# Kernel optimization log

Measured on AMD Instinct MI355X. Metric: run time of the kernel, lower is better.

The kernel has to match this reference:

```python
import jax, jax.numpy as jnp
import numpy as np

WS, OV, NH, CH = 16, 4, 6, 96
HD = CH // NH
SCALE = HD ** -0.5
EPS = 1e-5


def setup_inputs() -> dict:
    key = jax.random.key(0)
    ks = jax.random.split(key, 6)
    x = jax.random.normal(ks[0], (1, CH, 256, 256), jnp.float32)
    wq = jax.random.normal(ks[1], (CH, CH), jnp.float32) * 0.02      # torch Linear weight [out,in]
    wkv = jax.random.normal(ks[2], (2 * CH, CH), jnp.float32) * 0.02
    wproj = jax.random.normal(ks[3], (CH, CH), jnp.float32) * 0.02
    gamma = 1.0 + 0.02 * jax.random.normal(ks[4], (CH,), jnp.float32)
    beta = 0.02 * jax.random.normal(ks[5], (CH,), jnp.float32)
    return dict(x=x, wq=wq, wkv=wkv, wproj=wproj, gamma=gamma, beta=beta)


def reference(x, wq, wkv, wproj, gamma, beta):
    B, C, H, W = x.shape
    ws, ov, nh, hd = WS, OV, NH, HD
    ph = (ws - H % ws) % ws
    pw = (ws - W % ws) % ws
    xp = jnp.pad(x, ((0, 0), (0, 0), (0, ph), (0, pw)), mode='reflect') if (ph or pw) else x
    Hp, Wp = xp.shape[2], xp.shape[3]
    nhw, nww = Hp // ws, Wp // ws
    # non-overlapping query windows: (B*nW, ws*ws, C)
    xhw = xp.transpose(0, 2, 3, 1)  # B,Hp,Wp,C
    xwin = (xhw.reshape(B, nhw, ws, nww, ws, C)
                .transpose(0, 1, 3, 2, 4, 5)
                .reshape(B * nhw * nww, ws * ws, C))
    # LayerNorm (biased variance, eps=1e-5) then Q projection
    mu = xwin.mean(-1, keepdims=True)
    var = xwin.var(-1, keepdims=True)
    xn = (xwin - mu) / jnp.sqrt(var + EPS) * gamma + beta
    q = xn @ wq.T  # (Bw, ws*ws, C)
    # overlapping halo windows via gather (equiv. of pad + unfold)
    ws_ov = ws + 2 * ov
    xp2 = jnp.pad(xp, ((0, 0), (0, 0), (ov, ov), (ov, ov)), mode='reflect')
    ih = (jnp.arange(nhw) * ws)[:, None] + jnp.arange(ws_ov)[None, :]  # (nhw, ws_ov)
    iw = (jnp.arange(nww) * ws)[:, None] + jnp.arange(ws_ov)[None, :]  # (nww, ws_ov)
    xuf = xp2[:, :, ih[:, :, None, None], iw[None, None, :, :]]  # B,C,nhw,ws_ov,nww,ws_ov
    xuf = xuf.transpose(0, 2, 4, 3, 5, 1).reshape(B * nhw * nww, ws_ov * ws_ov, C)
    # KV projection and head split
    kv = (xuf @ wkv.T).reshape(-1, ws_ov * ws_ov, 2, nh, hd)
    k = kv[:, :, 0].transpose(0, 2, 1, 3)  # (Bw, nh, L2, hd)
    v = kv[:, :, 1].transpose(0, 2, 1, 3)
    qh = q.reshape(-1, ws * ws, nh, hd).transpose(0, 2, 1, 3)  # (Bw, nh, L1, hd)
    attn = jax.nn.softmax(jnp.einsum('bhqd,bhkd->bhqk', qh, k) * SCALE, axis=-1)
    out = jnp.einsum('bhqk,bhkd->bhqd', attn, v).transpose(0, 2, 1, 3).reshape(-1, ws * ws, C)
    out = out @ wproj.T + xwin
    out = (out.reshape(B, nhw, nww, ws, ws, C)
               .transpose(0, 1, 3, 2, 4, 5)
               .reshape(B, Hp, Wp, C)
               .transpose(0, 3, 1, 2))
    return out[:, :, :H, :W]
```

## Files before the change

kernel.cpp:

```cpp
#include <hip/hip_runtime.h>

#define NPIX 65536
#define HD 16
#define NTOK 576
#define QS 0.36067376022f
#define XPAD 100

typedef short s16x4 __attribute__((ext_vector_type(4)));
typedef short s16x8 __attribute__((ext_vector_type(8)));
typedef float f32x4 __attribute__((ext_vector_type(4)));

#define MFMA32(A, B, Cc) __builtin_amdgcn_mfma_f32_16x16x32_bf16((A), (B), (Cc), 0, 0, 0)

static __device__ __forceinline__ unsigned short f2b_rne(float f) {
    unsigned u = __builtin_bit_cast(unsigned, f);
    unsigned r = u + 0x7fffu + ((u >> 16) & 1u);
    return (unsigned short)(r >> 16);
}
static __device__ __forceinline__ float fexp2(float x) {
#if defined(__has_builtin)
#if __has_builtin(__builtin_amdgcn_exp2f)
    return __builtin_amdgcn_exp2f(x);
#else
    return exp2f(x);
#endif
#else
    return exp2f(x);
#endif
}
static __device__ __forceinline__ unsigned pkbf(float hi, float lo) {
#if defined(__has_builtin)
#if __has_builtin(__builtin_amdgcn_perm)
    return __builtin_amdgcn_perm(__builtin_bit_cast(unsigned, hi),
                                 __builtin_bit_cast(unsigned, lo), 0x07060302u);
#else
    return (__builtin_bit_cast(unsigned, hi) & 0xffff0000u) |
           (__builtin_bit_cast(unsigned, lo) >> 16);
#endif
#else
    return (__builtin_bit_cast(unsigned, hi) & 0xffff0000u) |
           (__builtin_bit_cast(unsigned, lo) >> 16);
#endif
}
static __device__ __forceinline__ int reflect_idx(int p) {
    p = (p < 0) ? -p : p;
    p = (p > 255) ? (510 - p) : p;
    return p;
}

__global__ __launch_bounds__(256) void prep_w(const float* __restrict__ wq,
                                              const float* __restrict__ wkv,
                                              const float* __restrict__ wproj,
                                              unsigned short* __restrict__ wB,
                                              unsigned short* __restrict__ wpB) {
    int idx = blockIdx.x * 256 + threadIdx.x;
    if (idx < 27648) {
        float v = (idx < 9216) ? wq[idx] : wkv[idx - 9216];
        wB[idx] = f2b_rne(v);
    } else {
        wpB[idx - 27648] = f2b_rne(wproj[idx - 27648]);
    }
}

__global__ __launch_bounds__(256, 2) void lnqkv(const float* __restrict__ x,
                                                const unsigned short* __restrict__ wB,
                                                const float* __restrict__ gamma,
                                                const float* __restrict__ beta,
                                                unsigned short* __restrict__ qwin,
                                                unsigned short* __restrict__ kmap,
                                                unsigned short* __restrict__ vmap) {
    __shared__ unsigned short xq[64][XPAD];
    __shared__ unsigned short xkv[64][XPAD];
    __shared__ float ps[4][64], pss[4][64];
    const int tid = threadIdx.x, lane = tid & 63, w = tid >> 6;
    const int p0 = blockIdx.x * 64;

    float xv[24];
    float s = 0.f, ss = 0.f;
#pragma unroll
    for (int i = 0; i < 24; ++i) {
        float v = x[(size_t)(w * 24 + i) * NPIX + p0 + lane];
        xv[i] = v; s += v; ss += v * v;
    }
    ps[w][lane] = s; pss[w][lane] = ss;
    __syncthreads();
    float st = 0.f, sst = 0.f;
#pragma unroll
    for (int q = 0; q < 4; ++q) { st += ps[q][lane]; sst += pss[q][lane]; }
    float mu = st * (1.0f / 96.0f);
    float var = sst * (1.0f / 96.0f) - mu * mu;
    float rs = rsqrtf(var + 1e-5f);
#pragma unroll
    for (int i = 0; i < 24; i += 2) {
        int c = w * 24 + i;
        float n0 = (xv[i] - mu) * rs * gamma[c] + beta[c];
        float n1 = (xv[i + 1] - mu) * rs * gamma[c + 1] + beta[c + 1];
        unsigned pq = (unsigned)f2b_rne(n0) | ((unsigned)f2b_rne(n1) << 16);
        *(unsigned*)&xq[lane][c] = pq;
        unsigned pk = (unsigned)f2b_rne(xv[i]) | ((unsigned)f2b_rne(xv[i + 1]) << 16);
        *(unsigned*)&xkv[lane][c] = pk;
    }
    __syncthreads();

    const int cq = lane & 15, g = lane >> 4;
    const int prow = w * 16 + cq;

    s16x8 bq[3], bkv[3];
#pragma unroll
    for (int ks = 0; ks < 3; ++ks) {
        int off = ks * 32 + g * 8;
        s16x4 lo = *(const s16x4*)&xq[prow][off];
        s16x4 hi = *(const s16x4*)&xq[prow][off + 4];
        bq[ks] = s16x8{lo[0], lo[1], lo[2], lo[3], hi[0], hi[1], hi[2], hi[3]};
        s16x4 lo2 = *(const s16x4*)&xkv[prow][off];
        s16x4 hi2 = *(const s16x4*)&xkv[prow][off + 4];
        bkv[ks] = s16x8{lo2[0], lo2[1], lo2[2], lo2[3], hi2[0], hi2[1], hi2[2], hi2[3]};
    }

    f32x4 acc[18];
#pragma unroll
    for (int t = 0; t < 18; ++t) acc[t] = f32x4{0.f, 0.f, 0.f, 0.f};
#pragma unroll
    for (int t = 0; t < 18; ++t) {
        const unsigned short* wrow = wB + (size_t)(t * 16 + cq) * 96 + g * 8;
        s16x8 a0 = *(const s16x8*)(wrow);
        s16x8 a1 = *(const s16x8*)(wrow + 32);
        s16x8 a2 = *(const s16x8*)(wrow + 64);
        if (t < 6) {
            acc[t] = MFMA32(a0, bq[0], acc[t]);
            acc[t] = MFMA32(a1, bq[1], acc[t]);
            acc[t] = MFMA32(a2, bq[2], acc[t]);
        } else {
            acc[t] = MFMA32(a0, bkv[0], acc[t]);
            acc[t] = MFMA32(a1, bkv[1], acc[t]);
            acc[t] = MFMA32(a2, bkv[2], acc[t]);
        }
    }

    const int p = p0 + prow;
    const int y = p >> 8, xx = p & 255;
    const int win = (y >> 4) * 16 + (xx >> 4);
    const int tok = (y & 15) * 16 + (xx & 15);
#pragma unroll
    for (int t = 0; t < 6; ++t) {
        union { s16x4 v; unsigned short h[4]; } u;
#pragma unroll
        for (int r = 0; r < 4; ++r) u.h[r] = f2b_rne(acc[t][r] * QS);
        *(s16x4*)(qwin + (size_t)(win * 256 + tok) * 96 + t * 16 + g * 4) = u.v;
    }
#pragma unroll
    for (int t = 6; t < 18; ++t) {
        int h = (t < 12) ? (t - 6) : (t - 12);
        unsigned short* base = (t < 12) ? kmap : vmap;
        union { s16x4 v; unsigned short h4[4]; } u;
#pragma unroll
        for (int r = 0; r < 4; ++r) u.h4[r] = f2b_rne(acc[t][r]);
        *(s16x4*)(base + (size_t)h * NPIX * HD + (size_t)p * HD + g * 4) = u.v;
    }
}

__global__ __launch_bounds__(256, 4) void attn_k(const unsigned short* __restrict__ qwin,
                                                 const unsigned short* __restrict__ kmap,
                                                 const unsigned short* __restrict__ vmap,
                                                 unsigned short* __restrict__ attn2) {
    __shared__ __align__(16) unsigned short vT_lds[16][580];
    __shared__ int koff[NTOK];
    const int tid = threadIdx.x;
    const int win = blockIdx.x / 6, head = blockIdx.x % 6;
    const int wi = win >> 4, wj = win & 15;

    const unsigned short* kbase = kmap + (size_t)head * NPIX * HD;
    const unsigned short* vbase = vmap + (size_t)head * NPIX * HD;
    for (int i = tid; i < NTOK; i += 256) {
        int r = i / 24, cc = i - r * 24;
        int py = reflect_idx(wi * 16 - 4 + r);
        int px = reflect_idx(wj * 16 - 4 + cc);
        int pix = py * 256 + px;
        koff[i] = pix * 32;
        const uint4* vsrc = (const uint4*)(vbase + (size_t)pix * HD);
        union { uint4 u; unsigned short h[8]; } ua, ub;
        ua.u = vsrc[0]; ub.u = vsrc[1];
#pragma unroll
        for (int d = 0; d < 8; ++d) vT_lds[d][i] = ua.h[d];
#pragma unroll
        for (int d = 0; d < 8; ++d) vT_lds[8 + d][i] = ub.h[d];
    }
    __syncthreads();

    const int lane = tid & 63, wv = tid >> 6;
    const int c = lane & 15, g = lane >> 4;
    const char* kbyte = (const char*)kbase + g * 8;

    union U8 { s16x8 v8; s16x4 v4[2]; };
    U8 qf[4];
#pragma unroll
    for (int qt = 0; qt < 4; ++qt) {
        int tok = wv * 64 + qt * 16 + c;
        qf[qt].v4[0] = *(const s16x4*)(qwin + ((size_t)(win * 256 + tok)) * 96 + head * HD + g * 4);
        qf[qt].v4[1] = s16x4{0, 0, 0, 0};
    }

    f32x4 o[4];
    float psA[4], psB[4];
#pragma unroll
    for (int qt = 0; qt < 4; ++qt) {
        o[qt] = f32x4{0.f, 0.f, 0.f, 0.f};
        psA[qt] = 0.f; psB[qt] = 0.f;
    }
    const f32x4 zero = f32x4{0.f, 0.f, 0.f, 0.f};

    U8 kf0, kf1, vf;
    kf0.v4[1] = s16x4{0, 0, 0, 0};
    kf1.v4[1] = s16x4{0, 0, 0, 0};

    for (int nt = 0; nt < 18; ++nt) {
        const int t0 = nt * 32;
        int o0 = koff[t0 + c];
        int o1 = koff[t0 + 16 + c];
        kf0.v4[0] = *(const s16x4*)(kbyte + o0);
        kf1.v4[0] = *(const s16x4*)(kbyte + o1);
        vf.v4[0] = *(const s16x4*)&vT_lds[c][t0 + g * 4];
        vf.v4[1] = *(const s16x4*)&vT_lds[c][t0 + 16 + g * 4];
#pragma unroll
        for (int qt = 0; qt < 4; ++qt) {
            f32x4 s0 = MFMA32(kf0.v8, qf[qt].v8, zero);
            f32x4 s1 = MFMA32(kf1.v8, qf[qt].v8, zero);
            float pe0 = fexp2(s0[0]), pe1 = fexp2(s0[1]);
            float pe2 = fexp2(s0[2]), pe3 = fexp2(s0[3]);
            float pe4 = fexp2(s1[0]), pe5 = fexp2(s1[1]);
            float pe6 = fexp2(s1[2]), pe7 = fexp2(s1[3]);
            psA[qt] += (pe0 + pe1) + (pe2 + pe3);
            psB[qt] += (pe4 + pe5) + (pe6 + pe7);
            union { uint4 u; s16x8 v; } bp;
            bp.u.x = pkbf(pe1, pe0);
            bp.u.y = pkbf(pe3, pe2);
            bp.u.z = pkbf(pe5, pe4);
            bp.u.w = pkbf(pe7, pe6);
            o[qt] = MFMA32(vf.v8, bp.v, o[qt]);
        }
    }

#pragma unroll
    for (int qt = 0; qt < 4; ++qt) {
        float d = psA[qt] + psB[qt];
        d += __shfl_xor(d, 16);
        d += __shfl_xor(d, 32);
        float inv = 1.0f / d;
        int tok = wv * 64 + qt * 16 + c;
        union { s16x4 v; unsigned short h[4]; } u;
#pragma unroll
        for (int r = 0; r < 4; ++r) u.h[r] = f2b_rne(o[qt][r] * inv);
        *(s16x4*)(attn2 + (size_t)(win * 256 + tok) * 96 + head * HD + g * 4) = u.v;
    }
}

__global__ __launch_bounds__(256) void proj_k(const unsigned short* __restrict__ attn2,
                                              const unsigned short* __restrict__ wpB,
                                              const float* __restrict__ x,
                                              float* __restrict__ out) {
    const int tid = threadIdx.x, lane = tid & 63, w = tid >> 6;
    const int cq = lane & 15, g = lane >> 4;
    const int p0 = blockIdx.x * 64;
    const int p = p0 + w * 16 + cq;
    const int y = p >> 8, xx = p & 255;
    const int win = (y >> 4) * 16 + (xx >> 4);
    const int tok = (y & 15) * 16 + (xx & 15);

    const unsigned short* arow = attn2 + (size_t)(win * 256 + tok) * 96 + g * 8;
    s16x8 b0 = *(const s16x8*)(arow);
    s16x8 b1 = *(const s16x8*)(arow + 32);
    s16x8 b2 = *(const s16x8*)(arow + 64);

    f32x4 acc[6];
#pragma unroll
    for (int t = 0; t < 6; ++t) acc[t] = f32x4{0.f, 0.f, 0.f, 0.f};
#pragma unroll
    for (int t = 0; t < 6; ++t) {
        const unsigned short* wrow = wpB + (size_t)(t * 16 + cq) * 96 + g * 8;
        acc[t] = MFMA32(*(const s16x8*)(wrow), b0, acc[t]);
        acc[t] = MFMA32(*(const s16x8*)(wrow + 32), b1, acc[t]);
        acc[t] = MFMA32(*(const s16x8*)(wrow + 64), b2, acc[t]);
    }
#pragma unroll
    for (int t = 0; t < 6; ++t) {
#pragma unroll
        for (int r = 0; r < 4; ++r) {
            size_t idx = (size_t)(t * 16 + 4 * g + r) * NPIX + p;
            out[idx] = acc[t][r] + x[idx];
        }
    }
}

extern "C" void kernel_launch(void* const* d_in, const int* in_sizes, int n_in,
                              void* d_out, int out_size, void* d_ws, size_t ws_size,
                              hipStream_t stream) {
    const float* x     = (const float*)d_in[0];
    const float* wq    = (const float*)d_in[1];
    const float* wkv   = (const float*)d_in[2];
    const float* wproj = (const float*)d_in[3];
    const float* gamma = (const float*)d_in[4];
    const float* beta  = (const float*)d_in[5];
    float* out = (float*)d_out;

    char* ws = (char*)d_ws;
    unsigned short* wB   = (unsigned short*)ws;
    unsigned short* wpB  = (unsigned short*)(ws + 55296);
    const size_t MAP = (size_t)NPIX * 96 * 2;
    unsigned short* qwin  = (unsigned short*)(ws + 73728);
    unsigned short* kmap  = (unsigned short*)(ws + 73728 + MAP);
    unsigned short* vmap  = (unsigned short*)(ws + 73728 + 2 * MAP);
    unsigned short* attn2 = (unsigned short*)(ws + 73728 + 3 * MAP);

    prep_w<<<144, 256, 0, stream>>>(wq, wkv, wproj, wB, wpB);
    lnqkv<<<1024, 256, 0, stream>>>(x, wB, gamma, beta, qwin, kmap, vmap);
    attn_k<<<1536, 256, 0, stream>>>(qwin, kmap, vmap, attn2);
    proj_k<<<1024, 256, 0, stream>>>(attn2, wpB, x, out);
}
```

Before: 86.11 us.

## Software-pipeline attention loop to overlap QK MFMA with exp and PV

Restructures the attention inner loop into a software pipeline. Each iteration issues the QK score MFMAs for the current tile, the PV MFMA for the previous tile, and prefetches the next tile's K and V, all before running exp/pack on the current scores. The aim is to hide MFMA and gather latency behind transcendental work. The koff and vT arrays are padded so the one-tile-ahead prefetch stays in bounds, at the cost of more registers for the buffered scores and probabilities under a 4-wave occupancy bound.

```diff
diff --git a/kernel.cpp b/kernel.cpp
--- a/kernel.cpp
+++ b/kernel.cpp
@@ -5,6 +5,7 @@
 #define NTOK 576
 #define QS 0.36067376022f
 #define XPAD 100
+#define VCOL 628
 
 typedef short s16x4 __attribute__((ext_vector_type(4)));
 typedef short s16x8 __attribute__((ext_vector_type(8)));
@@ -163,27 +164,31 @@
                                                  const unsigned short* __restrict__ kmap,
                                                  const unsigned short* __restrict__ vmap,
                                                  unsigned short* __restrict__ attn2) {
-    __shared__ __align__(16) unsigned short vT_lds[16][580];
-    __shared__ int koff[NTOK];
+    __shared__ __align__(16) unsigned short vT_lds[16][VCOL];
+    __shared__ int koff[640];
     const int tid = threadIdx.x;
     const int win = blockIdx.x / 6, head = blockIdx.x % 6;
     const int wi = win >> 4, wj = win & 15;
 
     const unsigned short* kbase = kmap + (size_t)head * NPIX * HD;
     const unsigned short* vbase = vmap + (size_t)head * NPIX * HD;
-    for (int i = tid; i < NTOK; i += 256) {
-        int r = i / 24, cc = i - r * 24;
-        int py = reflect_idx(wi * 16 - 4 + r);
-        int px = reflect_idx(wj * 16 - 4 + cc);
-        int pix = py * 256 + px;
-        koff[i] = pix * 32;
-        const uint4* vsrc = (const uint4*)(vbase + (size_t)pix * HD);
-        union { uint4 u; unsigned short h[8]; } ua, ub;
-        ua.u = vsrc[0]; ub.u = vsrc[1];
-#pragma unroll
-        for (int d = 0; d < 8; ++d) vT_lds[d][i] = ua.h[d];
-#pragma unroll
-        for (int d = 0; d < 8; ++d) vT_lds[8 + d][i] = ub.h[d];
+    for (int i = tid; i < 640; i += 256) {
+        if (i < NTOK) {
+            int r = i / 24, cc = i - r * 24;
+            int py = reflect_idx(wi * 16 - 4 + r);
+            int px = reflect_idx(wj * 16 - 4 + cc);
+            int pix = py * 256 + px;
+            koff[i] = pix * 32;
+            const uint4* vsrc = (const uint4*)(vbase + (size_t)pix * HD);
+            union { uint4 u; unsigned short h[8]; } ua, ub;
+            ua.u = vsrc[0]; ub.u = vsrc[1];
+#pragma unroll
+            for (int d = 0; d < 8; ++d) vT_lds[d][i] = ua.h[d];
+#pragma unroll
+            for (int d = 0; d < 8; ++d) vT_lds[8 + d][i] = ub.h[d];
+        } else {
+            koff[i] = 0;
+        }
     }
     __syncthreads();
 
@@ -212,33 +217,72 @@
     U8 kf0, kf1, vf;
     kf0.v4[1] = s16x4{0, 0, 0, 0};
     kf1.v4[1] = s16x4{0, 0, 0, 0};
-
-    for (int nt = 0; nt < 18; ++nt) {
-        const int t0 = nt * 32;
-        int o0 = koff[t0 + c];
-        int o1 = koff[t0 + 16 + c];
+    union BP { uint4 u; s16x8 v; } bp[4];
+
+    {
+        int o0 = koff[c], o1 = koff[16 + c];
         kf0.v4[0] = *(const s16x4*)(kbyte + o0);
         kf1.v4[0] = *(const s16x4*)(kbyte + o1);
-        vf.v4[0] = *(const s16x4*)&vT_lds[c][t0 + g * 4];
-        vf.v4[1] = *(const s16x4*)&vT_lds[c][t0 + 16 + g * 4];
+        vf.v4[0] = *(const s16x4*)&vT_lds[c][g * 4];
+        vf.v4[1] = *(const s16x4*)&vT_lds[c][16 + g * 4];
+    }
+    f32x4 s0[4], s1[4];
+#pragma unroll
+    for (int qt = 0; qt < 4; ++qt) {
+        s0[qt] = MFMA32(kf0.v8, qf[qt].v8, zero);
+        s1[qt] = MFMA32(kf1.v8, qf[qt].v8, zero);
+    }
+    {
+        int o0 = koff[32 + c], o1 = koff[48 + c];
+        kf0.v4[0] = *(const s16x4*)(kbyte + o0);
+        kf1.v4[0] = *(const s16x4*)(kbyte + o1);
+    }
+#pragma unroll
+    for (int qt = 0; qt < 4; ++qt) {
+        float pe0 = fexp2(s0[qt][0]), pe1 = fexp2(s0[qt][1]);
+        float pe2 = fexp2(s0[qt][2]), pe3 = fexp2(s0[qt][3]);
+        float pe4 = fexp2(s1[qt][0]), pe5 = fexp2(s1[qt][1]);
+        float pe6 = fexp2(s1[qt][2]), pe7 = fexp2(s1[qt][3]);
+        psA[qt] += (pe0 + pe1) + (pe2 + pe3);
+        psB[qt] += (pe4 + pe5) + (pe6 + pe7);
+        bp[qt].u.x = pkbf(pe1, pe0);
+        bp[qt].u.y = pkbf(pe3, pe2);
+        bp[qt].u.z = pkbf(pe5, pe4);
+        bp[qt].u.w = pkbf(pe7, pe6);
+    }
+
+    for (int nt = 1; nt < 18; ++nt) {
 #pragma unroll
         for (int qt = 0; qt < 4; ++qt) {
-            f32x4 s0 = MFMA32(kf0.v8, qf[qt].v8, zero);
-            f32x4 s1 = MFMA32(kf1.v8, qf[qt].v8, zero);
-            float pe0 = fexp2(s0[0]), pe1 = fexp2(s0[1]);
-            float pe2 = fexp2(s0[2]), pe3 = fexp2(s0[3]);
-            float pe4 = fexp2(s1[0]), pe5 = fexp2(s1[1]);
-            float pe6 = fexp2(s1[2]), pe7 = fexp2(s1[3]);
+            s0[qt] = MFMA32(kf0.v8, qf[qt].v8, zero);
+            s1[qt] = MFMA32(kf1.v8, qf[qt].v8, zero);
+        }
+#pragma unroll
+        for (int qt = 0; qt < 4; ++qt) o[qt] = MFMA32(vf.v8, bp[qt].v, o[qt]);
+        {
+            int o0 = koff[(nt + 1) * 32 + c], o1 = koff[(nt + 1) * 32 + 16 + c];
+            kf0.v4[0] = *(const s16x4*)(kbyte + o0);
+            kf1.v4[0] = *(const s16x4*)(kbyte + o1);
+            const int t0 = nt * 32;
+            vf.v4[0] = *(const s16x4*)&vT_lds[c][t0 + g * 4];
+            vf.v4[1] = *(const s16x4*)&vT_lds[c][t0 + 16 + g * 4];
+        }
+#pragma unroll
+        for (int qt = 0; qt < 4; ++qt) {
+            float pe0 = fexp2(s0[qt][0]), pe1 = fexp2(s0[qt][1]);
+            float pe2 = fexp2(s0[qt][2]), pe3 = fexp2(s0[qt][3]);
+            float pe4 = fexp2(s1[qt][0]), pe5 = fexp2(s1[qt][1]);
+            float pe6 = fexp2(s1[qt][2]), pe7 = fexp2(s1[qt][3]);
             psA[qt] += (pe0 + pe1) + (pe2 + pe3);
             psB[qt] += (pe4 + pe5) + (pe6 + pe7);
-            union { uint4 u; s16x8 v; } bp;
-            bp.u.x = pkbf(pe1, pe0);
-            bp.u.y = pkbf(pe3, pe2);
-            bp.u.z = pkbf(pe5, pe4);
-            bp.u.w = pkbf(pe7, pe6);
-            o[qt] = MFMA32(vf.v8, bp.v, o[qt]);
-        }
-    }
+            bp[qt].u.x = pkbf(pe1, pe0);
+            bp[qt].u.y = pkbf(pe3, pe2);
+            bp[qt].u.z = pkbf(pe5, pe4);
+            bp[qt].u.w = pkbf(pe7, pe6);
+        }
+    }
+#pragma unroll
+    for (int qt = 0; qt < 4; ++qt) o[qt] = MFMA32(vf.v8, bp[qt].v, o[qt]);
 
 #pragma unroll
     for (int qt = 0; qt < 4; ++qt) {
```

Measured after the change: 83.46 us. 3.1% less time.

## Software-pipeline K/V fragment loads in attention loop and swizzle block order

Applied to the files above, without the earlier changes.

Restructures the attention inner loop into double-buffered A/B stages that prefetch K fragments and key offsets two iterations ahead and V fragments from LDS, so global-load latency can overlap with MFMA and exp work. All score MFMAs for a stage are batched before the exponentials, and s_setprio raises wave priority around the MFMA groups. It also remaps blockIdx with an 8-way swizzle to change which windows and heads run together, and pads the LDS arrays so over-the-end prefetches read zeroed offsets and stay in bounds. The changes raise register pressure and LDS use per block, which could reduce occupancy.

```diff
diff --git a/kernel.cpp b/kernel.cpp
--- a/kernel.cpp
+++ b/kernel.cpp
@@ -5,6 +5,8 @@
 #define NTOK 576
 #define QS 0.36067376022f
 #define XPAD 100
+#define VCOL 692
+#define KOFFN 704
 
 typedef short s16x4 __attribute__((ext_vector_type(4)));
 typedef short s16x8 __attribute__((ext_vector_type(8)));
@@ -163,27 +165,32 @@
                                                  const unsigned short* __restrict__ kmap,
                                                  const unsigned short* __restrict__ vmap,
                                                  unsigned short* __restrict__ attn2) {
-    __shared__ __align__(16) unsigned short vT_lds[16][580];
-    __shared__ int koff[NTOK];
+    __shared__ __align__(16) unsigned short vT_lds[16][VCOL];
+    __shared__ int koff[KOFFN];
     const int tid = threadIdx.x;
-    const int win = blockIdx.x / 6, head = blockIdx.x % 6;
+    const int swz = (blockIdx.x & 7) * 192 + (blockIdx.x >> 3);
+    const int win = swz / 6, head = swz % 6;
     const int wi = win >> 4, wj = win & 15;
 
     const unsigned short* kbase = kmap + (size_t)head * NPIX * HD;
     const unsigned short* vbase = vmap + (size_t)head * NPIX * HD;
-    for (int i = tid; i < NTOK; i += 256) {
-        int r = i / 24, cc = i - r * 24;
-        int py = reflect_idx(wi * 16 - 4 + r);
-        int px = reflect_idx(wj * 16 - 4 + cc);
-        int pix = py * 256 + px;
-        koff[i] = pix * 32;
-        const uint4* vsrc = (const uint4*)(vbase + (size_t)pix * HD);
-        union { uint4 u; unsigned short h[8]; } ua, ub;
-        ua.u = vsrc[0]; ub.u = vsrc[1];
-#pragma unroll
-        for (int d = 0; d < 8; ++d) vT_lds[d][i] = ua.h[d];
-#pragma unroll
-        for (int d = 0; d < 8; ++d) vT_lds[8 + d][i] = ub.h[d];
+    for (int i = tid; i < KOFFN; i += 256) {
+        if (i < NTOK) {
+            int r = i / 24, cc = i - r * 24;
+            int py = reflect_idx(wi * 16 - 4 + r);
+            int px = reflect_idx(wj * 16 - 4 + cc);
+            int pix = py * 256 + px;
+            koff[i] = pix * 32;
+            const uint4* vsrc = (const uint4*)(vbase + (size_t)pix * HD);
+            union { uint4 u; unsigned short h[8]; } ua, ub;
+            ua.u = vsrc[0]; ub.u = vsrc[1];
+#pragma unroll
+            for (int d = 0; d < 8; ++d) vT_lds[d][i] = ua.h[d];
+#pragma unroll
+            for (int d = 0; d < 8; ++d) vT_lds[8 + d][i] = ub.h[d];
+        } else {
+            koff[i] = 0;
+        }
     }
     __syncthreads();
 
@@ -209,36 +216,63 @@
     }
     const f32x4 zero = f32x4{0.f, 0.f, 0.f, 0.f};
 
-    U8 kf0, kf1, vf;
-    kf0.v4[1] = s16x4{0, 0, 0, 0};
-    kf1.v4[1] = s16x4{0, 0, 0, 0};
-
-    for (int nt = 0; nt < 18; ++nt) {
-        const int t0 = nt * 32;
-        int o0 = koff[t0 + c];
-        int o1 = koff[t0 + 16 + c];
-        kf0.v4[0] = *(const s16x4*)(kbyte + o0);
-        kf1.v4[0] = *(const s16x4*)(kbyte + o1);
-        vf.v4[0] = *(const s16x4*)&vT_lds[c][t0 + g * 4];
-        vf.v4[1] = *(const s16x4*)&vT_lds[c][t0 + 16 + g * 4];
-#pragma unroll
-        for (int qt = 0; qt < 4; ++qt) {
-            f32x4 s0 = MFMA32(kf0.v8, qf[qt].v8, zero);
-            f32x4 s1 = MFMA32(kf1.v8, qf[qt].v8, zero);
-            float pe0 = fexp2(s0[0]), pe1 = fexp2(s0[1]);
-            float pe2 = fexp2(s0[2]), pe3 = fexp2(s0[3]);
-            float pe4 = fexp2(s1[0]), pe5 = fexp2(s1[1]);
-            float pe6 = fexp2(s1[2]), pe7 = fexp2(s1[3]);
-            psA[qt] += (pe0 + pe1) + (pe2 + pe3);
-            psB[qt] += (pe4 + pe5) + (pe6 + pe7);
-            union { uint4 u; s16x8 v; } bp;
-            bp.u.x = pkbf(pe1, pe0);
-            bp.u.y = pkbf(pe3, pe2);
-            bp.u.z = pkbf(pe5, pe4);
-            bp.u.w = pkbf(pe7, pe6);
-            o[qt] = MFMA32(vf.v8, bp.v, o[qt]);
-        }
-    }
+    U8 kf0A, kf1A, vfA, kf0B, kf1B, vfB;
+    kf0A.v4[1] = s16x4{0, 0, 0, 0};
+    kf1A.v4[1] = s16x4{0, 0, 0, 0};
+    kf0B.v4[1] = s16x4{0, 0, 0, 0};
+    kf1B.v4[1] = s16x4{0, 0, 0, 0};
+
+    kf0A.v4[0] = *(const s16x4*)(kbyte + koff[c]);
+    kf1A.v4[0] = *(const s16x4*)(kbyte + koff[16 + c]);
+    kf0B.v4[0] = *(const s16x4*)(kbyte + koff[32 + c]);
+    kf1B.v4[0] = *(const s16x4*)(kbyte + koff[48 + c]);
+    vfA.v4[0] = *(const s16x4*)&vT_lds[c][g * 4];
+    vfA.v4[1] = *(const s16x4*)&vT_lds[c][16 + g * 4];
+    vfB.v4[0] = *(const s16x4*)&vT_lds[c][32 + g * 4];
+    vfB.v4[1] = *(const s16x4*)&vT_lds[c][48 + g * 4];
+    int oA0 = koff[64 + c],  oA1 = koff[80 + c];
+    int oB0 = koff[96 + c],  oB1 = koff[112 + c];
+
+#define BODY(KF0, KF1, VF, O0, O1, NTPF, NTOFF) do {                          \
+    f32x4 s0[4], s1[4];                                                       \
+    __builtin_amdgcn_s_setprio(1);                                            \
+    _Pragma("unroll")                                                         \
+    for (int qt = 0; qt < 4; ++qt) {                                          \
+        s0[qt] = MFMA32(KF0.v8, qf[qt].v8, zero);                             \
+        s1[qt] = MFMA32(KF1.v8, qf[qt].v8, zero);                             \
+    }                                                                         \
+    __builtin_amdgcn_s_setprio(0);                                            \
+    KF0.v4[0] = *(const s16x4*)(kbyte + O0);                  \
+    KF1.v4[0] = *(const s16x4*)(kbyte + O1);                                  \
+    O0 = koff[(NTOFF) * 32 + c];                           \
+    O1 = koff[(NTOFF) * 32 + 16 + c];                                         \
+    union { uint4 u; s16x8 v; } bp[4];                                        \
+    _Pragma("unroll")                                                         \
+    for (int qt = 0; qt < 4; ++qt) {                                          \
+        float pe0 = fexp2(s0[qt][0]), pe1 = fexp2(s0[qt][1]);                 \
+        float pe2 = fexp2(s0[qt][2]), pe3 = fexp2(s0[qt][3]);                 \
+        float pe4 = fexp2(s1[qt][0]), pe5 = fexp2(s1[qt][1]);                 \
+        float pe6 = fexp2(s1[qt][2]), pe7 = fexp2(s1[qt][3]);                 \
+        psA[qt] += (pe0 + pe1) + (pe2 + pe3);                                 \
+        psB[qt] += (pe4 + pe5) + (pe6 + pe7);                                 \
+        bp[qt].u.x = pkbf(pe1, pe0);                                          \
+        bp[qt].u.y = pkbf(pe3, pe2);                                          \
+        bp[qt].u.z = pkbf(pe5, pe4);                                          \
+        bp[qt].u.w = pkbf(pe7, pe6);                                          \
+    }                                                                         \
+    __builtin_amdgcn_s_setprio(1);                                            \
+    _Pragma("unroll")                                                         \
+    for (int qt = 0; qt < 4; ++qt) o[qt] = MFMA32(VF.v8, bp[qt].v, o[qt]);    \
+    __builtin_amdgcn_s_setprio(0);                                            \
+    VF.v4[0] = *(const s16x4*)&vT_lds[c][(NTPF) * 32 + g * 4];                \
+    VF.v4[1] = *(const s16x4*)&vT_lds[c][(NTPF) * 32 + 16 + g * 4];           \
+} while (0)
+
+    for (int nt = 0; nt < 18; nt += 2) {
+        BODY(kf0A, kf1A, vfA, oA0, oA1, nt + 2, nt + 4);
+        BODY(kf0B, kf1B, vfB, oB0, oB1, nt + 3, nt + 5);
+    }
+#undef BODY
 
 #pragma unroll
     for (int qt = 0; qt < 4; ++qt) {
```

New measurement: 150.4 us. +74.7%, slower.
